# Kernel optimization log

Hardware: AMD Instinct MI355X
Metric: run time of the kernel (lower is better)

The kernel has to match this reference:

```python
import jax, jax.numpy as jnp
import numpy as np

N = 50000        # num nodes
E = 600000       # num edges (before self-loops)
EPS = 1e-5       # BatchNorm eps


def _norm_coeffs(edge_index):
    # PyG GCNConv normalization: add self-loops, symmetric deg^-1/2 norm.
    loop = jnp.arange(N, dtype=edge_index.dtype)
    src = jnp.concatenate([edge_index[0], loop])
    dst = jnp.concatenate([edge_index[1], loop])
    deg = jax.ops.segment_sum(jnp.ones(src.shape[0], jnp.float32), dst, num_segments=N)
    dis = jax.lax.rsqrt(jnp.maximum(deg, 1.0))  # deg >= 1 due to self-loops
    norm = dis[src] * dis[dst]                  # [E+N]
    return src, dst, norm


def _gcn_layer(h, W, b, src, dst, norm):
    h = h @ W                                   # dense transform [N, out]
    msg = h[src] * norm[:, None]                # gather + scale  [E+N, out]
    agg = jax.ops.segment_sum(msg, dst, num_segments=N)  # scatter-add
    return agg + b


def _bn_relu(h, gamma, beta):
    mean = jnp.mean(h, axis=0)
    var = jnp.var(h, axis=0)
    h = (h - mean) * jax.lax.rsqrt(var + EPS) * gamma + beta
    return jax.nn.relu(h)


def setup_inputs() -> dict:
    key = jax.random.key(0)
    ks = jax.random.split(key, 5)
    x = jax.random.normal(ks[0], (N, 128), jnp.float32)
    edge_index = jax.random.randint(ks[1], (2, E), 0, N, jnp.int64)
    s = 0.05
    return {
        "x": x,
        "edge_index": edge_index,
        "W1": jax.random.normal(ks[2], (128, 128), jnp.float32) * s,
        "b1": jnp.zeros((128,), jnp.float32),
        "gamma1": jnp.ones((128,), jnp.float32),
        "beta1": jnp.zeros((128,), jnp.float32),
        "W2": jax.random.normal(ks[3], (128, 128), jnp.float32) * s,
        "b2": jnp.zeros((128,), jnp.float32),
        "gamma2": jnp.ones((128,), jnp.float32),
        "beta2": jnp.zeros((128,), jnp.float32),
        "W3": jax.random.normal(ks[4], (128, 64), jnp.float32) * s,
        "b3": jnp.zeros((64,), jnp.float32),
    }


def reference(x, edge_index, W1, b1, gamma1, beta1, W2, b2, gamma2, beta2, W3, b3):
    src, dst, norm = _norm_coeffs(edge_index)
    h = _gcn_layer(x, W1, b1, src, dst, norm)
    h = _bn_relu(h, gamma1, beta1)
    h = _gcn_layer(h, W2, b2, src, dst, norm)
    h = _bn_relu(h, gamma2, beta2)
    return _gcn_layer(h, W3, b3, src, dst, norm)
```

## Files before the change

### kernel.cpp

```cpp
#include <hip/hip_runtime.h>
#include <hip/hip_bf16.h>


#define NCHUNK 1024
#define NSLOT 64
#define NPW 4

typedef short bf16x8 __attribute__((ext_vector_type(8)));
typedef float f32x4 __attribute__((ext_vector_type(4)));

union FragU { uint4 u; bf16x8 f; };

static __device__ __forceinline__ float4 ld4(const float* p) {
    return *reinterpret_cast<const float4*>(p);
}

static __device__ __forceinline__ unsigned pk2(float lo, float hi) {
    __hip_bfloat162 h = __float22bfloat162_rn(make_float2(lo, hi));
    union { __hip_bfloat162 h2; unsigned u; } c;
    c.h2 = h;
    return c.u;
}
static __device__ __forceinline__ unsigned short bf1(float v) {
    return (unsigned short)(pk2(v, 0.f) & 0xffffu);
}
static __device__ __forceinline__ float bf_lo(unsigned u) { return __uint_as_float(u << 16); }
static __device__ __forceinline__ float bf_hi(unsigned u) { return __uint_as_float(u & 0xffff0000u); }

__global__ __launch_bounds__(256) void k_setup(int* __restrict__ cnt,
                                               float* __restrict__ stats, int n,
                                               int gbInit,
                                               const float* __restrict__ W1,
                                               const float* __restrict__ W2,
                                               const float* __restrict__ W3,
                                               unsigned short* __restrict__ wf1,
                                               unsigned short* __restrict__ wf2,
                                               unsigned short* __restrict__ wf3) {
    int b = blockIdx.x;
    if (b < gbInit) {
        int i = b * 256 + threadIdx.x;
        if (i < n) cnt[i] = 0;
        if (i < 4 * NSLOT * 128) stats[i] = 0.f;
        return;
    }
    int unit = (b - gbInit) * 4 + (threadIdx.x >> 6);
    if (unit >= 80) return;
    int l = threadIdx.x & 63;
    const float* W; unsigned short* Wf; int NC; int blk;
    if (unit < 32)      { W = W1; Wf = wf1; NC = 128; blk = unit; }
    else if (unit < 64) { W = W2; Wf = wf2; NC = 128; blk = unit - 32; }
    else                { W = W3; Wf = wf3; NC = 64;  blk = unit - 64; }
    int kk = blk & 3;
    int col = (blk >> 2) * 16 + (l & 15);
    int k0 = kk * 32 + (l >> 4) * 8;
    unsigned short* dst = &Wf[((size_t)blk * 64 + l) * 8];
#pragma unroll
    for (int j = 0; j < 8; ++j)
        dst[j] = bf1(W[(size_t)(k0 + j) * NC + col]);
}

__global__ void k_count(const int* __restrict__ dst, int* __restrict__ cnt, int e) {
    int i = blockIdx.x * 256 + threadIdx.x;
    if (i < e) atomicAdd(&cnt[dst[i]], 1);
}

__global__ __launch_bounds__(256) void k_chunksum(const int* __restrict__ cnt,
                                                  int* __restrict__ chunkSum, int n) {
    int t = blockIdx.x * 256 + threadIdx.x;
    int per = (n + NCHUNK - 1) / NCHUNK;
    int lo = t * per; if (lo > n) lo = n;
    int hi = lo + per; if (hi > n) hi = n;
    int s = 0;
    for (int i = lo; i < hi; ++i) s += cnt[i];
    chunkSum[t] = s;
}

__global__ __launch_bounds__(256) void k_chunkwrite(const int* __restrict__ cnt,
                                                    const int* __restrict__ chunkSum,
                                                    int* __restrict__ offs,
                                                    int* __restrict__ cursor,
                                                    float* __restrict__ dis,
                                                    int n, int e) {
    __shared__ int lbase[NCHUNK];
    __shared__ int lth[256];
    int t = threadIdx.x;
    int a0 = chunkSum[t * 4 + 0], a1 = chunkSum[t * 4 + 1];
    int a2 = chunkSum[t * 4 + 2], a3 = chunkSum[t * 4 + 3];
    lth[t] = a0 + a1 + a2 + a3;
    __syncthreads();
    for (int off = 1; off < 256; off <<= 1) {
        int v = (t >= off) ? lth[t - off] : 0;
        __syncthreads();
        lth[t] += v;
        __syncthreads();
    }
    int base = (t == 0) ? 0 : lth[t - 1];
    lbase[t * 4 + 0] = base;
    lbase[t * 4 + 1] = base + a0;
    lbase[t * 4 + 2] = base + a0 + a1;
    lbase[t * 4 + 3] = base + a0 + a1 + a2;
    __syncthreads();
    int cid = blockIdx.x * 256 + t;
    int per = (n + NCHUNK - 1) / NCHUNK;
    int lo = cid * per; if (lo > n) lo = n;
    int hi = lo + per; if (hi > n) hi = n;
    int run = lbase[cid];
    for (int i = lo; i < hi; ++i) {
        offs[i] = run;
        cursor[i] = run;
        int c = cnt[i];
        dis[i] = rsqrtf((float)(c + 1));
        run += c;
    }
    if (cid == 0) offs[n] = e;
}

__global__ void k_scatter(const int* __restrict__ src, const int* __restrict__ dst,
                          int* __restrict__ cursor, int* __restrict__ csr, int e) {
    int i = blockIdx.x * 256 + threadIdx.x;
    if (i < e) {
        int p = atomicAdd(&cursor[dst[i]], 1);
        csr[p] = src[i];
    }
}

template <bool TRANS, int NC, bool INBF>
__global__ __launch_bounds__(256) void k_gemm(const void* __restrict__ inv,
                                              const uint4* __restrict__ Wf,
                                              const float* __restrict__ dis,
                                              const float* __restrict__ ta,
                                              const float* __restrict__ tc,
                                              unsigned short* __restrict__ out, int n) {
    constexpr int TPW = NC / 32;
    constexpr int PADC = NC + 8;
    constexpr int SHN = (32 * PADC > 32 * 128) ? 32 * PADC : 32 * 128;
    __shared__ unsigned short sh[SHN];
    const int tid = threadIdx.x;
    const int row0 = blockIdx.x * 32;

    if constexpr (INBF) {
        const unsigned short* in = (const unsigned short*)inv;
#pragma unroll
        for (int it = 0; it < 2; ++it) {
            int flat = it * 256 + tid;
            int r = flat >> 4, j = flat & 15;
            int grow = row0 + r;
            uint4 v = make_uint4(0, 0, 0, 0);
            if (grow < n) v = *reinterpret_cast<const uint4*>(&in[(size_t)grow * 128 + j * 8]);
            if (TRANS) {
                int f = j * 8;
                float4 A0 = ld4(&ta[f]), A1 = ld4(&ta[f + 4]);
                float4 C0 = ld4(&tc[f]), C1 = ld4(&tc[f + 4]);
                v.x = pk2(fmaxf(bf_lo(v.x) * A0.x + C0.x, 0.f),
                          fmaxf(bf_hi(v.x) * A0.y + C0.y, 0.f));
                v.y = pk2(fmaxf(bf_lo(v.y) * A0.z + C0.z, 0.f),
                          fmaxf(bf_hi(v.y) * A0.w + C0.w, 0.f));
                v.z = pk2(fmaxf(bf_lo(v.z) * A1.x + C1.x, 0.f),
                          fmaxf(bf_hi(v.z) * A1.y + C1.y, 0.f));
                v.w = pk2(fmaxf(bf_lo(v.w) * A1.z + C1.z, 0.f),
                          fmaxf(bf_hi(v.w) * A1.w + C1.w, 0.f));
            }
            int byte = r * 256 + ((j * 16) ^ ((r & 7) << 4));
            *reinterpret_cast<uint4*>(reinterpret_cast<char*>(sh) + byte) = v;
        }
    } else {
        const float* in = (const float*)inv;
#pragma unroll
        for (int it = 0; it < 4; ++it) {
            int flat = it * 256 + tid;
            int r = flat >> 5, j4 = flat & 31;
            int grow = row0 + r;
            float4 v = make_float4(0.f, 0.f, 0.f, 0.f);
            if (grow < n) v = ld4(&in[(size_t)grow * 128 + j4 * 4]);
            if (TRANS) {
                int f = j4 * 4;
                float4 A = ld4(&ta[f]);
                float4 C = ld4(&tc[f]);
                v.x = fmaxf(v.x * A.x + C.x, 0.f);
                v.y = fmaxf(v.y * A.y + C.y, 0.f);
                v.z = fmaxf(v.z * A.z + C.z, 0.f);
                v.w = fmaxf(v.w * A.w + C.w, 0.f);
            }
            int byte = r * 256 + ((j4 * 8) ^ ((r & 7) << 4));
            *reinterpret_cast<uint2*>(reinterpret_cast<char*>(sh) + byte) =
                make_uint2(pk2(v.x, v.y), pk2(v.z, v.w));
        }
    }
    __syncthreads();

    const int l = tid & 63, w = tid >> 6;
    const int l15 = l & 15, g = l >> 4;
    const int rhalf = (w >> 1) * 16;
    const int tbase = (w & 1) * TPW;

    f32x4 acc[TPW];
#pragma unroll
    for (int t = 0; t < TPW; ++t) acc[t] = (f32x4){0.f, 0.f, 0.f, 0.f};

    const int arow = rhalf + l15;
    const char* xb = reinterpret_cast<const char*>(sh) + arow * 256;
    const int aswz = (arow & 7) << 4;

#pragma unroll
    for (int kk = 0; kk < 4; ++kk) {
        FragU a;
        a.u = *reinterpret_cast<const uint4*>(xb + ((kk * 64 + g * 16) ^ aswz));
#pragma unroll
        for (int t = 0; t < TPW; ++t) {
            FragU b;
            b.u = Wf[(size_t)((tbase + t) * 4 + kk) * 64 + l];
            acc[t] = __builtin_amdgcn_mfma_f32_16x16x32_bf16(a.f, b.f, acc[t], 0, 0, 0);
        }
    }

    const int rbase = row0 + rhalf + g * 4;
    float dv[4];
#pragma unroll
    for (int r = 0; r < 4; ++r) {
        int rr = rbase + r;
        dv[r] = (rr < n) ? dis[rr] : 0.f;
    }
    __syncthreads();
#pragma unroll
    for (int t = 0; t < TPW; ++t) {
        int col = (tbase + t) * 16 + l15;
#pragma unroll
        for (int r = 0; r < 4; ++r) {
            int lrow = rhalf + g * 4 + r;
            sh[lrow * PADC + col] = bf1(acc[t][r] * dv[r]);
        }
    }
    __syncthreads();
    constexpr int U4R = NC / 8;
#pragma unroll
    for (int it = 0; it < (32 * U4R) / 256; ++it) {
        int flat = it * 256 + tid;
        int row = flat / U4R, j = flat % U4R;
        int grow = row0 + row;
        if (grow < n) {
            uint4 v = *reinterpret_cast<const uint4*>(&sh[row * PADC + j * 8]);
            *reinterpret_cast<uint4*>(&out[(size_t)grow * NC + j * 8]) = v;
        }
    }
}

template <int NC, bool STATS>
__global__ __launch_bounds__(256) void k_agg(const unsigned short* __restrict__ hs,
                                             const int* __restrict__ offs,
                                             const int* __restrict__ csr,
                                             const float* __restrict__ dis,
                                             const float* __restrict__ bias,
                                             void* __restrict__ outv,
                                             float* __restrict__ ssum,
                                             float* __restrict__ ssq, int n) {
    const int wave = threadIdx.x >> 6, lane = threadIdx.x & 63;
    const int half = lane >> 5, l32 = lane & 31;
    const int nodeBase = blockIdx.x * (4 * NPW) + wave * NPW;

    float4 st = make_float4(0.f, 0.f, 0.f, 0.f);
    float4 sq = make_float4(0.f, 0.f, 0.f, 0.f);

    for (int j = 0; j < NPW; ++j) {
        const int node = nodeBase + j;
        int e0 = 0, e1 = 0;
        if (node < n) { e0 = offs[node]; e1 = offs[node + 1]; }

        if (NC == 128) {
            const uint2* hp = reinterpret_cast<const uint2*>(hs);
            float4 a0 = make_float4(0.f, 0.f, 0.f, 0.f);
            float4 a1 = a0, a2 = a0, a3 = a0;
            if (half == 0 && node < n) {
                uint2 w = hp[(size_t)node * 32 + l32];
                a0 = make_float4(bf_lo(w.x), bf_hi(w.x), bf_lo(w.y), bf_hi(w.y));
            }
            int e = e0;
            for (; e + 8 <= e1; e += 8) {
                int i0 = csr[e + 0 + half];
                int i1 = csr[e + 2 + half];
                int i2 = csr[e + 4 + half];
                int i3 = csr[e + 6 + half];
                uint2 w0 = hp[(size_t)i0 * 32 + l32];
                uint2 w1 = hp[(size_t)i1 * 32 + l32];
                uint2 w2 = hp[(size_t)i2 * 32 + l32];
                uint2 w3 = hp[(size_t)i3 * 32 + l32];
                a0.x += bf_lo(w0.x); a0.y += bf_hi(w0.x); a0.z += bf_lo(w0.y); a0.w += bf_hi(w0.y);
                a1.x += bf_lo(w1.x); a1.y += bf_hi(w1.x); a1.z += bf_lo(w1.y); a1.w += bf_hi(w1.y);
                a2.x += bf_lo(w2.x); a2.y += bf_hi(w2.x); a2.z += bf_lo(w2.y); a2.w += bf_hi(w2.y);
                a3.x += bf_lo(w3.x); a3.y += bf_hi(w3.x); a3.z += bf_lo(w3.y); a3.w += bf_hi(w3.y);
            }
            for (; e + 2 <= e1; e += 2) {
                int i0 = csr[e + half];
                uint2 w0 = hp[(size_t)i0 * 32 + l32];
                a0.x += bf_lo(w0.x); a0.y += bf_hi(w0.x); a0.z += bf_lo(w0.y); a0.w += bf_hi(w0.y);
            }
            if (e < e1 && half == 0) {
                int i0 = csr[e];
                uint2 w0 = hp[(size_t)i0 * 32 + l32];
                a0.x += bf_lo(w0.x); a0.y += bf_hi(w0.x); a0.z += bf_lo(w0.y); a0.w += bf_hi(w0.y);
            }
            a0.x += a1.x + a2.x + a3.x;
            a0.y += a1.y + a2.y + a3.y;
            a0.z += a1.z + a2.z + a3.z;
            a0.w += a1.w + a2.w + a3.w;
            a0.x += __shfl_down(a0.x, 32);
            a0.y += __shfl_down(a0.y, 32);
            a0.z += __shfl_down(a0.z, 32);
            a0.w += __shfl_down(a0.w, 32);
            if (half == 0 && node < n) {
                float d = dis[node];
                float4 b = ld4(&bias[l32 * 4]);
                float4 oV = make_float4(d * a0.x + b.x, d * a0.y + b.y,
                                        d * a0.z + b.z, d * a0.w + b.w);
                uint2 w = make_uint2(pk2(oV.x, oV.y), pk2(oV.z, oV.w));
                reinterpret_cast<uint2*>(outv)[(size_t)node * 32 + l32] = w;
                if (STATS) {
                    st.x += oV.x; sq.x += oV.x * oV.x;
                    st.y += oV.y; sq.y += oV.y * oV.y;
                    st.z += oV.z; sq.z += oV.z * oV.z;
                    st.w += oV.w; sq.w += oV.w * oV.w;
                }
            }
        } else {
            const unsigned* hp = reinterpret_cast<const unsigned*>(hs);
            float2 a0 = make_float2(0.f, 0.f);
            float2 a1 = a0, a2 = a0, a3 = a0;
            if (half == 0 && node < n) {
                unsigned w = hp[(size_t)node * 32 + l32];
                a0 = make_float2(bf_lo(w), bf_hi(w));
            }
            int e = e0;
            for (; e + 8 <= e1; e += 8) {
                int i0 = csr[e + 0 + half];
                int i1 = csr[e + 2 + half];
                int i2 = csr[e + 4 + half];
                int i3 = csr[e + 6 + half];
                unsigned w0 = hp[(size_t)i0 * 32 + l32];
                unsigned w1 = hp[(size_t)i1 * 32 + l32];
                unsigned w2 = hp[(size_t)i2 * 32 + l32];
                unsigned w3 = hp[(size_t)i3 * 32 + l32];
                a0.x += bf_lo(w0); a0.y += bf_hi(w0);
                a1.x += bf_lo(w1); a1.y += bf_hi(w1);
                a2.x += bf_lo(w2); a2.y += bf_hi(w2);
                a3.x += bf_lo(w3); a3.y += bf_hi(w3);
            }
            for (; e + 2 <= e1; e += 2) {
                int i0 = csr[e + half];
                unsigned w0 = hp[(size_t)i0 * 32 + l32];
                a0.x += bf_lo(w0); a0.y += bf_hi(w0);
            }
            if (e < e1 && half == 0) {
                int i0 = csr[e];
                unsigned w0 = hp[(size_t)i0 * 32 + l32];
                a0.x += bf_lo(w0); a0.y += bf_hi(w0);
            }
            a0.x += a1.x + a2.x + a3.x;
            a0.y += a1.y + a2.y + a3.y;
            a0.x += __shfl_down(a0.x, 32);
            a0.y += __shfl_down(a0.y, 32);
            if (half == 0 && node < n) {
                float d = dis[node];
                float2 o = make_float2(d * a0.x + bias[l32 * 2],
                                       d * a0.y + bias[l32 * 2 + 1]);
                reinterpret_cast<float2*>(outv)[(size_t)node * 32 + l32] = o;
            }
        }
    }

    if constexpr (STATS) {
        __shared__ float ls[4][128];
        __shared__ float ls2[4][128];
        if (half == 0) {
            int c = l32 * 4;
            ls[wave][c + 0] = st.x; ls2[wave][c + 0] = sq.x;
            ls[wave][c + 1] = st.y; ls2[wave][c + 1] = sq.y;
            ls[wave][c + 2] = st.z; ls2[wave][c + 2] = sq.z;
            ls[wave][c + 3] = st.w; ls2[wave][c + 3] = sq.w;
        }
        __syncthreads();
        int t = threadIdx.x;
        int slot = (blockIdx.x & (NSLOT - 1)) * 128;
        if (t < 128) {
            atomicAdd(&ssum[slot + t], ls[0][t] + ls[1][t] + ls[2][t] + ls[3][t]);
        } else {
            int c = t - 128;
            atomicAdd(&ssq[slot + c], ls2[0][c] + ls2[1][c] + ls2[2][c] + ls2[3][c]);
        }
    }
}

__global__ void k_bnparams(const float* __restrict__ ssum, const float* __restrict__ ssq,
                           const float* __restrict__ gamma, const float* __restrict__ beta,
                           float* __restrict__ a, float* __restrict__ cc, int n) {
    int c = threadIdx.x;
    if (c < 128) {
        float s = 0.f, s2 = 0.f;
        for (int k = 0; k < NSLOT; ++k) {
            s += ssum[k * 128 + c];
            s2 += ssq[k * 128 + c];
        }
        float inv_n = 1.0f / (float)n;
        float mean = s * inv_n;
        float var = s2 * inv_n - mean * mean;
        float sc = gamma[c] * rsqrtf(var + 1e-5f);
        a[c] = sc;
        cc[c] = beta[c] - mean * sc;
    }
}

extern "C" void kernel_launch(void* const* d_in, const int* in_sizes, int n_in,
                              void* d_out, int out_size, void* d_ws, size_t ws_size,
                              hipStream_t stream) {
    const float* x      = (const float*)d_in[0];
    const int*   ei     = (const int*)d_in[1];
    const float* W1     = (const float*)d_in[2];
    const float* b1     = (const float*)d_in[3];
    const float* gamma1 = (const float*)d_in[4];
    const float* beta1  = (const float*)d_in[5];
    const float* W2     = (const float*)d_in[6];
    const float* b2     = (const float*)d_in[7];
    const float* gamma2 = (const float*)d_in[8];
    const float* beta2  = (const float*)d_in[9];
    const float* W3     = (const float*)d_in[10];
    const float* b3     = (const float*)d_in[11];
    float* out = (float*)d_out;

    const int n = in_sizes[0] / 128;
    const int e = in_sizes[1] / 2;
    const int* esrc = ei;
    const int* edst = ei + e;

    char* p = (char*)d_ws;
    auto alloc = [&](size_t bytes) {
        void* r = p;
        p += (bytes + 255) & ~size_t(255);
        return r;
    };
    unsigned short* hbf  = (unsigned short*)alloc(sizeof(unsigned short) * (size_t)n * 128);
    unsigned short* bufB = (unsigned short*)alloc(sizeof(unsigned short) * (size_t)n * 128);
    int*   cnt    = (int*)alloc(sizeof(int) * n);
    int*   offs   = (int*)alloc(sizeof(int) * (n + 1));
    int*   cursor = (int*)alloc(sizeof(int) * n);
    int*   csr    = (int*)alloc(sizeof(int) * e);
    float* dis    = (float*)alloc(sizeof(float) * n);
    float* stats  = (float*)alloc(sizeof(float) * 4 * NSLOT * 128);
    float* bn     = (float*)alloc(sizeof(float) * 512);
    int*   chunkSum = (int*)alloc(sizeof(int) * NCHUNK);
    unsigned short* wf1 = (unsigned short*)alloc(sizeof(unsigned short) * 32 * 64 * 8);
    unsigned short* wf2 = (unsigned short*)alloc(sizeof(unsigned short) * 32 * 64 * 8);
    unsigned short* wf3 = (unsigned short*)alloc(sizeof(unsigned short) * 16 * 64 * 8);
    float* ssum1 = stats,                   *ssq1 = stats + NSLOT * 128;
    float* ssum2 = stats + 2 * NSLOT * 128, *ssq2 = stats + 3 * NSLOT * 128;
    float* a1 = bn, *cc1 = bn + 128, *a2 = bn + 256, *cc2 = bn + 384;

    int gb_n  = (n + 255) / 256;
    int gb_e  = (e + 255) / 256;
    int gb_gemm = (n + 31) / 32;
    int gb_agg = (n + 4 * NPW - 1) / (4 * NPW);

    k_setup<<<gb_n + 20, 256, 0, stream>>>(cnt, stats, n, gb_n, W1, W2, W3, wf1, wf2, wf3);
    k_count<<<gb_e, 256, 0, stream>>>(edst, cnt, e);
    k_chunksum<<<NCHUNK / 256, 256, 0, stream>>>(cnt, chunkSum, n);
    k_chunkwrite<<<NCHUNK / 256, 256, 0, stream>>>(cnt, chunkSum, offs, cursor, dis, n, e);
    k_scatter<<<gb_e, 256, 0, stream>>>(esrc, edst, cursor, csr, e);

    k_gemm<false, 128, false><<<gb_gemm, 256, 0, stream>>>(x, (const uint4*)wf1, dis, nullptr, nullptr, hbf, n);
    k_agg<128, true><<<gb_agg, 256, 0, stream>>>(hbf, offs, csr, dis, b1, bufB, ssum1, ssq1, n);
    k_bnparams<<<1, 128, 0, stream>>>(ssum1, ssq1, gamma1, beta1, a1, cc1, n);

    k_gemm<true, 128, true><<<gb_gemm, 256, 0, stream>>>(bufB, (const uint4*)wf2, dis, a1, cc1, hbf, n);
    k_agg<128, true><<<gb_agg, 256, 0, stream>>>(hbf, offs, csr, dis, b2, bufB, ssum2, ssq2, n);
    k_bnparams<<<1, 128, 0, stream>>>(ssum2, ssq2, gamma2, beta2, a2, cc2, n);

    k_gemm<true, 64, true><<<gb_gemm, 256, 0, stream>>>(bufB, (const uint4*)wf3, dis, a2, cc2, hbf, n);
    k_agg<64, false><<<gb_agg, 256, 0, stream>>>(hbf, offs, csr, dis, b3, out, nullptr, nullptr, n);
}
```

Measured before the change: 245.2 us.

## Fuse BN parameter computation into aggregation via last-block counter; predicate edge tails

Removes the two single-block k_bnparams launches. The last block of each stats-producing aggregation kernel, found with an atomic counter and fences, now reduces the per-slot sums into BN scale and shift. The edge loop is also rewritten as one 8-wide loop with clamped indices and predicated accumulation, replacing the separate remainder loops. This cuts two launches and some tail divergence, but adds a fence and atomic per block and redundant gathers on partial iterations.

Measured after the change: 781.9 us. 3.19x slower.

```diff
diff --git a/kernel.cpp b/kernel.cpp
--- a/kernel.cpp
+++ b/kernel.cpp
@@ -28,7 +28,8 @@
 static __device__ __forceinline__ float bf_hi(unsigned u) { return __uint_as_float(u & 0xffff0000u); }
 
 __global__ __launch_bounds__(256) void k_setup(int* __restrict__ cnt,
-                                               float* __restrict__ stats, int n,
+                                               float* __restrict__ stats,
+                                               int* __restrict__ counters, int n,
                                                int gbInit,
                                                const float* __restrict__ W1,
                                                const float* __restrict__ W2,
@@ -41,6 +42,7 @@
         int i = b * 256 + threadIdx.x;
         if (i < n) cnt[i] = 0;
         if (i < 4 * NSLOT * 128) stats[i] = 0.f;
+        if (i < 8) counters[i] = 0;
         return;
     }
     int unit = (b - gbInit) * 4 + (threadIdx.x >> 6);
@@ -252,7 +254,12 @@
                                              const float* __restrict__ bias,
                                              void* __restrict__ outv,
                                              float* __restrict__ ssum,
-                                             float* __restrict__ ssq, int n) {
+                                             float* __restrict__ ssq,
+                                             const float* __restrict__ gamma,
+                                             const float* __restrict__ beta,
+                                             float* __restrict__ aOut,
+                                             float* __restrict__ ccOut,
+                                             int* __restrict__ counter, int n) {
     const int wave = threadIdx.x >> 6, lane = threadIdx.x & 63;
     const int half = lane >> 5, l32 = lane & 31;
     const int nodeBase = blockIdx.x * (4 * NPW) + wave * NPW;
@@ -273,30 +280,22 @@
                 uint2 w = hp[(size_t)node * 32 + l32];
                 a0 = make_float4(bf_lo(w.x), bf_hi(w.x), bf_lo(w.y), bf_hi(w.y));
             }
-            int e = e0;
-            for (; e + 8 <= e1; e += 8) {
-                int i0 = csr[e + 0 + half];
-                int i1 = csr[e + 2 + half];
-                int i2 = csr[e + 4 + half];
-                int i3 = csr[e + 6 + half];
+            const int lim = e1 - 1;
+            for (int e = e0; e < e1; e += 8) {
+                int ee0 = e + 0 + half, ee1 = e + 2 + half;
+                int ee2 = e + 4 + half, ee3 = e + 6 + half;
+                int i0 = csr[ee0 <= lim ? ee0 : lim];
+                int i1 = csr[ee1 <= lim ? ee1 : lim];
+                int i2 = csr[ee2 <= lim ? ee2 : lim];
+                int i3 = csr[ee3 <= lim ? ee3 : lim];
                 uint2 w0 = hp[(size_t)i0 * 32 + l32];
                 uint2 w1 = hp[(size_t)i1 * 32 + l32];
                 uint2 w2 = hp[(size_t)i2 * 32 + l32];
                 uint2 w3 = hp[(size_t)i3 * 32 + l32];
-                a0.x += bf_lo(w0.x); a0.y += bf_hi(w0.x); a0.z += bf_lo(w0.y); a0.w += bf_hi(w0.y);
-                a1.x += bf_lo(w1.x); a1.y += bf_hi(w1.x); a1.z += bf_lo(w1.y); a1.w += bf_hi(w1.y);
-                a2.x += bf_lo(w2.x); a2.y += bf_hi(w2.x); a2.z += bf_lo(w2.y); a2.w += bf_hi(w2.y);
-                a3.x += bf_lo(w3.x); a3.y += bf_hi(w3.x); a3.z += bf_lo(w3.y); a3.w += bf_hi(w3.y);
-            }
-            for (; e + 2 <= e1; e += 2) {
-                int i0 = csr[e + half];
-                uint2 w0 = hp[(size_t)i0 * 32 + l32];
-                a0.x += bf_lo(w0.x); a0.y += bf_hi(w0.x); a0.z += bf_lo(w0.y); a0.w += bf_hi(w0.y);
-            }
-            if (e < e1 && half == 0) {
-                int i0 = csr[e];
-                uint2 w0 = hp[(size_t)i0 * 32 + l32];
-                a0.x += bf_lo(w0.x); a0.y += bf_hi(w0.x); a0.z += bf_lo(w0.y); a0.w += bf_hi(w0.y);
+                if (ee0 < e1) { a0.x += bf_lo(w0.x); a0.y += bf_hi(w0.x); a0.z += bf_lo(w0.y); a0.w += bf_hi(w0.y); }
+                if (ee1 < e1) { a1.x += bf_lo(w1.x); a1.y += bf_hi(w1.x); a1.z += bf_lo(w1.y); a1.w += bf_hi(w1.y); }
+                if (ee2 < e1) { a2.x += bf_lo(w2.x); a2.y += bf_hi(w2.x); a2.z += bf_lo(w2.y); a2.w += bf_hi(w2.y); }
+                if (ee3 < e1) { a3.x += bf_lo(w3.x); a3.y += bf_hi(w3.x); a3.z += bf_lo(w3.y); a3.w += bf_hi(w3.y); }
             }
             a0.x += a1.x + a2.x + a3.x;
             a0.y += a1.y + a2.y + a3.y;
@@ -328,30 +327,22 @@
                 unsigned w = hp[(size_t)node * 32 + l32];
                 a0 = make_float2(bf_lo(w), bf_hi(w));
             }
-            int e = e0;
-            for (; e + 8 <= e1; e += 8) {
-                int i0 = csr[e + 0 + half];
-                int i1 = csr[e + 2 + half];
-                int i2 = csr[e + 4 + half];
-                int i3 = csr[e + 6 + half];
+            const int lim = e1 - 1;
+            for (int e = e0; e < e1; e += 8) {
+                int ee0 = e + 0 + half, ee1 = e + 2 + half;
+                int ee2 = e + 4 + half, ee3 = e + 6 + half;
+                int i0 = csr[ee0 <= lim ? ee0 : lim];
+                int i1 = csr[ee1 <= lim ? ee1 : lim];
+                int i2 = csr[ee2 <= lim ? ee2 : lim];
+                int i3 = csr[ee3 <= lim ? ee3 : lim];
                 unsigned w0 = hp[(size_t)i0 * 32 + l32];
                 unsigned w1 = hp[(size_t)i1 * 32 + l32];
                 unsigned w2 = hp[(size_t)i2 * 32 + l32];
                 unsigned w3 = hp[(size_t)i3 * 32 + l32];
-                a0.x += bf_lo(w0); a0.y += bf_hi(w0);
-                a1.x += bf_lo(w1); a1.y += bf_hi(w1);
-                a2.x += bf_lo(w2); a2.y += bf_hi(w2);
-                a3.x += bf_lo(w3); a3.y += bf_hi(w3);
-            }
-            for (; e + 2 <= e1; e += 2) {
-                int i0 = csr[e + half];
-                unsigned w0 = hp[(size_t)i0 * 32 + l32];
-                a0.x += bf_lo(w0); a0.y += bf_hi(w0);
-            }
-            if (e < e1 && half == 0) {
-                int i0 = csr[e];
-                unsigned w0 = hp[(size_t)i0 * 32 + l32];
-                a0.x += bf_lo(w0); a0.y += bf_hi(w0);
+                if (ee0 < e1) { a0.x += bf_lo(w0); a0.y += bf_hi(w0); }
+                if (ee1 < e1) { a1.x += bf_lo(w1); a1.y += bf_hi(w1); }
+                if (ee2 < e1) { a2.x += bf_lo(w2); a2.y += bf_hi(w2); }
+                if (ee3 < e1) { a3.x += bf_lo(w3); a3.y += bf_hi(w3); }
             }
             a0.x += a1.x + a2.x + a3.x;
             a0.y += a1.y + a2.y + a3.y;
@@ -369,6 +360,7 @@
     if constexpr (STATS) {
         __shared__ float ls[4][128];
         __shared__ float ls2[4][128];
+        __shared__ int sIsLast;
         if (half == 0) {
             int c = l32 * 4;
             ls[wave][c + 0] = st.x; ls2[wave][c + 0] = sq.x;
@@ -385,25 +377,31 @@
             int c = t - 128;
             atomicAdd(&ssq[slot + c], ls2[0][c] + ls2[1][c] + ls2[2][c] + ls2[3][c]);
         }
-    }
-}
-
-__global__ void k_bnparams(const float* __restrict__ ssum, const float* __restrict__ ssq,
-                           const float* __restrict__ gamma, const float* __restrict__ beta,
-                           float* __restrict__ a, float* __restrict__ cc, int n) {
-    int c = threadIdx.x;
-    if (c < 128) {
-        float s = 0.f, s2 = 0.f;
-        for (int k = 0; k < NSLOT; ++k) {
-            s += ssum[k * 128 + c];
-            s2 += ssq[k * 128 + c];
-        }
-        float inv_n = 1.0f / (float)n;
-        float mean = s * inv_n;
-        float var = s2 * inv_n - mean * mean;
-        float sc = gamma[c] * rsqrtf(var + 1e-5f);
-        a[c] = sc;
-        cc[c] = beta[c] - mean * sc;
+        __threadfence();
+        if (t == 0) {
+            int prev = __hip_atomic_fetch_add(counter, 1, __ATOMIC_ACQ_REL,
+                                              __HIP_MEMORY_SCOPE_AGENT);
+            sIsLast = (prev == (int)gridDim.x - 1) ? 1 : 0;
+        }
+        __syncthreads();
+        if (sIsLast) {
+            __threadfence();
+            if (t < 128) {
+                float s = 0.f, s2 = 0.f;
+                for (int k = 0; k < NSLOT; ++k) {
+                    s += __hip_atomic_load(&ssum[k * 128 + t], __ATOMIC_RELAXED,
+                                           __HIP_MEMORY_SCOPE_AGENT);
+                    s2 += __hip_atomic_load(&ssq[k * 128 + t], __ATOMIC_RELAXED,
+                                            __HIP_MEMORY_SCOPE_AGENT);
+                }
+                float inv_n = 1.0f / (float)n;
+                float mean = s * inv_n;
+                float var = s2 * inv_n - mean * mean;
+                float sc = gamma[t] * rsqrtf(var + 1e-5f);
+                aOut[t] = sc;
+                ccOut[t] = beta[t] - mean * sc;
+            }
+        }
     }
 }
 
@@ -444,6 +442,7 @@
     float* dis    = (float*)alloc(sizeof(float) * n);
     float* stats  = (float*)alloc(sizeof(float) * 4 * NSLOT * 128);
     float* bn     = (float*)alloc(sizeof(float) * 512);
+    int*   counters = (int*)alloc(sizeof(int) * 8);
     int*   chunkSum = (int*)alloc(sizeof(int) * NCHUNK);
     unsigned short* wf1 = (unsigned short*)alloc(sizeof(unsigned short) * 32 * 64 * 8);
     unsigned short* wf2 = (unsigned short*)alloc(sizeof(unsigned short) * 32 * 64 * 8);
@@ -457,20 +456,21 @@
     int gb_gemm = (n + 31) / 32;
     int gb_agg = (n + 4 * NPW - 1) / (4 * NPW);
 
-    k_setup<<<gb_n + 20, 256, 0, stream>>>(cnt, stats, n, gb_n, W1, W2, W3, wf1, wf2, wf3);
+    k_setup<<<gb_n + 20, 256, 0, stream>>>(cnt, stats, counters, n, gb_n, W1, W2, W3, wf1, wf2, wf3);
     k_count<<<gb_e, 256, 0, stream>>>(edst, cnt, e);
     k_chunksum<<<NCHUNK / 256, 256, 0, stream>>>(cnt, chunkSum, n);
     k_chunkwrite<<<NCHUNK / 256, 256, 0, stream>>>(cnt, chunkSum, offs, cursor, dis, n, e);
     k_scatter<<<gb_e, 256, 0, stream>>>(esrc, edst, cursor, csr, e);
 
     k_gemm<false, 128, false><<<gb_gemm, 256, 0, stream>>>(x, (const uint4*)wf1, dis, nullptr, nullptr, hbf, n);
-    k_agg<128, true><<<gb_agg, 256, 0, stream>>>(hbf, offs, csr, dis, b1, bufB, ssum1, ssq1, n);
-    k_bnparams<<<1, 128, 0, stream>>>(ssum1, ssq1, gamma1, beta1, a1, cc1, n);
+    k_agg<128, true><<<gb_agg, 256, 0, stream>>>(hbf, offs, csr, dis, b1, bufB,
+                                                 ssum1, ssq1, gamma1, beta1, a1, cc1, &counters[0], n);
 
     k_gemm<true, 128, true><<<gb_gemm, 256, 0, stream>>>(bufB, (const uint4*)wf2, dis, a1, cc1, hbf, n);
-    k_agg<128, true><<<gb_agg, 256, 0, stream>>>(hbf, offs, csr, dis, b2, bufB, ssum2, ssq2, n);
-    k_bnparams<<<1, 128, 0, stream>>>(ssum2, ssq2, gamma2, beta2, a2, cc2, n);
+    k_agg<128, true><<<gb_agg, 256, 0, stream>>>(hbf, offs, csr, dis, b2, bufB,
+                                                 ssum2, ssq2, gamma2, beta2, a2, cc2, &counters[1], n);
 
     k_gemm<true, 64, true><<<gb_gemm, 256, 0, stream>>>(bufB, (const uint4*)wf3, dis, a2, cc2, hbf, n);
-    k_agg<64, false><<<gb_agg, 256, 0, stream>>>(hbf, offs, csr, dis, b3, out, nullptr, nullptr, n);
-}
+    k_agg<64, false><<<gb_agg, 256, 0, stream>>>(hbf, offs, csr, dis, b3, out,
+                                                 nullptr, nullptr, nullptr, nullptr, nullptr, nullptr, &counters[2], n);
+}
```
